# Optimization experiments

Measured on AMD Instinct MI355X. Metric: run time of the kernel, lower is better.

Reference implementation:

```python
import jax, jax.numpy as jnp
import numpy as np

EMBED_DIM = 1024
NUM_HEADS = 16
HEAD_DIM = EMBED_DIM // NUM_HEADS
BATCH = 2
SEQ = 2048


def setup_inputs() -> dict:
    key = jax.random.key(0)
    ks = jax.random.split(key, 9)
    s = EMBED_DIM ** -0.5
    inp = {"x": jax.random.normal(ks[0], (BATCH, SEQ, EMBED_DIM), dtype=jnp.float32)}
    names = ["Wq", "Wk", "Wv", "Wo"]
    for i, n in enumerate(names):
        inp[n] = jax.random.normal(ks[1 + i], (EMBED_DIM, EMBED_DIM), dtype=jnp.float32) * s
        inp["b" + n[1]] = jax.random.normal(ks[5 + i], (EMBED_DIM,), dtype=jnp.float32) * 0.02
    return inp


def reference(x, Wq, bq, Wk, bk, Wv, bv, Wo, bo):
    B, S, E = x.shape
    H, D = NUM_HEADS, HEAD_DIM
    scaling = D ** -0.5
    # projections (torch Linear: x @ W.T + b), reshape to (B, H, S, D)
    q = (x @ Wq.T + bq).reshape(B, S, H, D).transpose(0, 2, 1, 3)
    k = (x @ Wk.T + bk).reshape(B, S, H, D).transpose(0, 2, 1, 3)
    v = (x @ Wv.T + bv).reshape(B, S, H, D).transpose(0, 2, 1, 3)
    # full materialized score matrix, matching the original module
    scores = jnp.einsum("bhqd,bhkd->bhqk", q, k) * scaling
    causal = jnp.triu(jnp.ones((S, S), dtype=bool), k=1)  # True above diagonal
    scores = jnp.where(causal[None, None], -jnp.inf, scores)
    attn = jax.nn.softmax(scores, axis=-1)
    out = jnp.einsum("bhqk,bhkd->bhqd", attn, v)  # (B, H, S, D)
    out = out.transpose(0, 2, 1, 3).reshape(B, S, E)
    return out @ Wo.T + bo
```

## Files before the change

kernel.cpp:

```cpp
#include <hip/hip_runtime.h>
#include <stdint.h>

typedef __bf16 bf16;
typedef __bf16 bf16x8 __attribute__((ext_vector_type(8)));
typedef __bf16 bf16x4 __attribute__((ext_vector_type(4)));
typedef float  f32x4  __attribute__((ext_vector_type(4)));
typedef unsigned int u32;

#define E_DIM 1024
#define S_LEN 2048
#define BATCH 2
#define NH 16
#define DH 64

#define NEG_INF (-__builtin_inff())

union BU { u32 u[4]; bf16x8 h; };

__device__ __forceinline__ u32 cvtpk_bf16(float lo, float hi) {
    u32 r;
    asm("v_cvt_pk_bf16_f32 %0, %1, %2" : "=v"(r) : "v"(lo), "v"(hi));
    return r;
}
__device__ __forceinline__ void pswap32(u32 &a, u32 &b) {
    asm("v_permlane32_swap_b32 %0, %1" : "+v"(a), "+v"(b));
}
__device__ __forceinline__ void pswap16(u32 &a, u32 &b) {
    asm("v_permlane16_swap_b32 %0, %1" : "+v"(a), "+v"(b));
}
__device__ __forceinline__ float fast_exp2(float x) {
    float r;
    asm("v_exp_f32 %0, %1" : "=v"(r) : "v"(x));
    return r;
}

__device__ __forceinline__ void load_lds16(const bf16* g, bf16* l) {
    __builtin_amdgcn_global_load_lds(
        (const __attribute__((address_space(1))) void*)g,
        (__attribute__((address_space(3))) void*)l, 16, 0, 0);
}

__global__ __launch_bounds__(256) void convert_kernel(
    const float* __restrict__ s0, const float* __restrict__ s1,
    const float* __restrict__ s2, const float* __restrict__ s3,
    const float* __restrict__ s4,
    bf16* __restrict__ d0, bf16* __restrict__ d1, bf16* __restrict__ d2,
    bf16* __restrict__ d3, bf16* __restrict__ d4,
    int n0, int n1)
{
    const float* src; bf16* dst; int n;
    switch (blockIdx.y) {
        case 0:  src = s0; dst = d0; n = n0; break;
        case 1:  src = s1; dst = d1; n = n1; break;
        case 2:  src = s2; dst = d2; n = n1; break;
        case 3:  src = s3; dst = d3; n = n1; break;
        default: src = s4; dst = d4; n = n1; break;
    }
    int i = (blockIdx.x * 256 + threadIdx.x) * 4;
    if (i >= n) return;
    float4 v = *(const float4*)(src + i);
    bf16x4 o;
    o[0] = (bf16)v.x; o[1] = (bf16)v.y; o[2] = (bf16)v.z; o[3] = (bf16)v.w;
    *(bf16x4*)(dst + i) = o;
}

__global__ __launch_bounds__(256) void gemm_kernel(
    const bf16* __restrict__ A,
    const bf16* __restrict__ W,
    const float* __restrict__ bias0, const float* __restrict__ bias1,
    const float* __restrict__ bias2,
    bf16* __restrict__ outQ, bf16* __restrict__ outK, bf16* __restrict__ outVt,
    float* __restrict__ outF, int final_mode)
{
    __shared__ bf16 As[2][128 * 32];
    __shared__ bf16 Bs[2][128 * 32];

    const int bid = blockIdx.x;
    const int xcd = bid & 7, idx = bid >> 3;
    int mtile, ntile;
    if (final_mode) {
        mtile = (xcd >> 1) * 8 + (idx >> 2);
        ntile = (xcd & 1) * 4 + (idx & 3);
    } else {
        mtile = (xcd >> 1) * 8 + idx / 12;
        ntile = (xcd & 1) * 12 + idx % 12;
    }
    const int bm = mtile * 128, bn = ntile * 128;
    const int mode = final_mode ? 3 : (bn >> 10);
    const float* bias = (mode == 1) ? bias1 : (mode == 2 ? bias2 : bias0);

    const int t = threadIdx.x;
    const int lane = t & 63, w = t >> 6;
    const int quad = lane >> 4, l16 = lane & 15;
    const int wm = (w & 1) * 64, wn = (w >> 1) * 64;

    const int r0 = w * 16;
    const int srow = r0 + (lane >> 2);
    const int scol = ((lane & 3) ^ ((lane >> 3) & 3)) * 8;
    const bf16* Ag0 = A + (size_t)(bm + srow) * E_DIM + scol;
    const bf16* Ag1 = Ag0 + (size_t)64 * E_DIM;
    const bf16* Wg0 = W + (size_t)(bn + srow) * E_DIM + scol;
    const bf16* Wg1 = Wg0 + (size_t)64 * E_DIM;

    f32x4 acc[4][4];
#pragma unroll
    for (int i = 0; i < 4; i++)
#pragma unroll
        for (int j = 0; j < 4; j++) acc[i][j] = f32x4{0.f, 0.f, 0.f, 0.f};

    load_lds16(Ag0, As[0] + r0 * 32);
    load_lds16(Ag1, As[0] + (64 + r0) * 32);
    load_lds16(Wg0, Bs[0] + r0 * 32);
    load_lds16(Wg1, Bs[0] + (64 + r0) * 32);

    const int rchunk = (quad ^ ((l16 >> 1) & 3)) * 8;

    int cur = 0;
    for (int kt = 0; kt < E_DIM; kt += 32) {
        __syncthreads();

        if (kt + 32 < E_DIM) {
            const int nxt = cur ^ 1;
            load_lds16(Ag0 + kt + 32, As[nxt] + r0 * 32);
            load_lds16(Ag1 + kt + 32, As[nxt] + (64 + r0) * 32);
            load_lds16(Wg0 + kt + 32, Bs[nxt] + r0 * 32);
            load_lds16(Wg1 + kt + 32, Bs[nxt] + (64 + r0) * 32);
        }

        bf16x8 af[4], bfr[4];
#pragma unroll
        for (int i = 0; i < 4; i++)
            af[i] = *(const bf16x8*)(As[cur] + (wm + i * 16 + l16) * 32 + rchunk);
#pragma unroll
        for (int j = 0; j < 4; j++)
            bfr[j] = *(const bf16x8*)(Bs[cur] + (wn + j * 16 + l16) * 32 + rchunk);
#pragma unroll
        for (int i = 0; i < 4; i++)
#pragma unroll
            for (int j = 0; j < 4; j++)
                acc[i][j] = __builtin_amdgcn_mfma_f32_16x16x32_bf16(af[i], bfr[j], acc[i][j], 0, 0, 0);

        cur ^= 1;
    }

#pragma unroll
    for (int j = 0; j < 4; j++) {
        const int n = bn + wn + j * 16 + l16;
        const int nl = n & 1023;
        const float bv = bias[nl];
#pragma unroll
        for (int i = 0; i < 4; i++) {
            const int m0 = bm + wm + i * 16 + quad * 4;
            if (mode == 3) {
#pragma unroll
                for (int r = 0; r < 4; r++)
                    outF[(size_t)(m0 + r) * E_DIM + nl] = acc[i][j][r] + bv;
            } else if (mode == 2) {
                const int b_ = m0 >> 11, s0 = m0 & (S_LEN - 1);
                const int h = nl >> 6, d = nl & 63;
                bf16x4 pv;
#pragma unroll
                for (int r = 0; r < 4; r++) pv[r] = (bf16)(acc[i][j][r] + bv);
                *(bf16x4*)(outVt + ((size_t)((b_ * NH + h) * DH + d)) * S_LEN + s0) = pv;
            } else {
                bf16* o = (mode == 0) ? outQ : outK;
                const float sc = (mode == 0) ? 0.18033688f : 1.0f;
                const int h = nl >> 6, d = nl & 63;
#pragma unroll
                for (int r = 0; r < 4; r++) {
                    const int m = m0 + r;
                    const int b_ = m >> 11, s = m & (S_LEN - 1);
                    o[((size_t)(b_ * NH + h) * S_LEN + s) * DH + d] = (bf16)((acc[i][j][r] + bv) * sc);
                }
            }
        }
    }
}

__global__ __launch_bounds__(512, 4) void attn_kernel(
    const bf16* __restrict__ Qb, const bf16* __restrict__ Kb,
    const bf16* __restrict__ Vtb,
    float* __restrict__ Opart, float* __restrict__ Lpart)
{
    __shared__ __align__(16) char smem[35840];
    bf16* Ks = (bf16*)smem;
    bf16* Vs = (bf16*)(smem + 18432);

    const int t = threadIdx.x, lane = t & 63, w = t >> 6;
    const int quad = lane >> 4, l16 = lane & 15;
    const int qs = w & 3, kh = w >> 2;

    const int i = blockIdx.x;
    const int xcd = i & 7, idx = i >> 3;
    const int bh  = (xcd << 2) | (idx & 3);
    const int g   = idx >> 2;
    int qt, c0;
    if (g < 4)       { qt = g;                            c0 = 0; }
    else if (g < 12) { int u = g - 4;  qt = 4 + (u >> 1); c0 = u & 1; }
    else if (g < 24) { int u = g - 12; qt = 8 + u / 3;    c0 = u % 3; }
    else             { int u = g - 24; qt = 12 + (u >> 2); c0 = u & 3; }
    const int k0 = c0 * 4;
    const int k1 = (k0 + 3 < qt) ? k0 + 3 : qt;

    const bf16* Qg = Qb + (size_t)bh * S_LEN * DH;
    const bf16* Kg = Kb + (size_t)bh * S_LEN * DH;
    const bf16* Vg = Vtb + (size_t)bh * DH * S_LEN;
    float* Op = Opart + ((size_t)(bh * 16 + qt) * 4 + c0) * (128 * 64);
    float* Lp = Lpart + ((size_t)(bh * 16 + qt) * 4 + c0) * 128;

    const int qrow0 = qt * 128 + qs * 32;

    bf16x8 qf[2][2];
#pragma unroll
    for (int qh = 0; qh < 2; qh++) {
        const bf16* qp = Qg + (size_t)(qrow0 + qh * 16 + l16) * DH + quad * 8;
        qf[qh][0] = *(const bf16x8*)(qp);
        qf[qh][1] = *(const bf16x8*)(qp + 32);
    }

    f32x4 o[2][4];
    f32x4 lacc[2];
#pragma unroll
    for (int qh = 0; qh < 2; qh++) {
        lacc[qh] = f32x4{0.f, 0.f, 0.f, 0.f};
#pragma unroll
        for (int dt = 0; dt < 4; dt++) o[qh][dt] = f32x4{0.f, 0.f, 0.f, 0.f};
    }

    const int kr0 = t >> 3, kce = (t & 7) * 8;
    const int vr0 = t >> 4, vce = (t & 15) * 8;

    const int kb0 = k0 * 128;
    uint4 kA = *(const uint4*)(Kg + (size_t)(kb0 + kr0) * DH + kce);
    uint4 kB = *(const uint4*)(Kg + (size_t)(kb0 + kr0 + 64) * DH + kce);
    uint4 vA = *(const uint4*)(Vg + (size_t)vr0 * S_LEN + kb0 + vce);
    uint4 vB = *(const uint4*)(Vg + (size_t)(vr0 + 32) * S_LEN + kb0 + vce);

    for (int kt = k0; kt <= k1; kt++) {
        __syncthreads();
        *(uint4*)(Ks + kr0 * 72 + kce) = kA;
        *(uint4*)(Ks + (kr0 + 64) * 72 + kce) = kB;
        *(uint4*)(Vs + vr0 * 136 + vce) = vA;
        *(uint4*)(Vs + (vr0 + 32) * 136 + vce) = vB;
        __syncthreads();

        if (kt < k1) {
            const int kb = (kt + 1) * 128;
            kA = *(const uint4*)(Kg + (size_t)(kb + kr0) * DH + kce);
            kB = *(const uint4*)(Kg + (size_t)(kb + kr0 + 64) * DH + kce);
            vA = *(const uint4*)(Vg + (size_t)vr0 * S_LEN + kb + vce);
            vB = *(const uint4*)(Vg + (size_t)(vr0 + 32) * S_LEN + kb + vce);
        }

        const bool diag = (kt == qt);

#pragma unroll
        for (int itp = 0; itp < 2; itp++) {
            f32x4 p[2][2];
#pragma unroll
            for (int e = 0; e < 2; e++) {
                const int itg = kh * 4 + itp * 2 + e;
                const bf16* kp = Ks + (itg * 16 + l16) * 72 + quad * 8;
                bf16x8 kf0 = *(const bf16x8*)(kp);
                bf16x8 kf1 = *(const bf16x8*)(kp + 32);
#pragma unroll
                for (int qh = 0; qh < 2; qh++) {
                    f32x4 s = __builtin_amdgcn_mfma_f32_16x16x32_bf16(
                        kf0, qf[qh][0], f32x4{0.f, 0.f, 0.f, 0.f}, 0, 0, 0);
                    s = __builtin_amdgcn_mfma_f32_16x16x32_bf16(
                        kf1, qf[qh][1], s, 0, 0, 0);
                    if (diag) {
                        const int kloc = kh * 64 + (itp * 2 + e) * 16 + quad * 4;
                        const int qloc = qs * 32 + qh * 16 + l16;
#pragma unroll
                        for (int r = 0; r < 4; r++)
                            if (kloc + r > qloc) s[r] = NEG_INF;
                    }
                    f32x4 pe;
#pragma unroll
                    for (int r = 0; r < 4; r++) pe[r] = fast_exp2(s[r]);
                    lacc[qh] += pe;
                    p[qh][e] = pe;
                }
            }

            BU bu0, bu1;
            {
                u32 a0 = cvtpk_bf16(p[0][0][0], p[0][0][1]);
                u32 a1 = cvtpk_bf16(p[0][0][2], p[0][0][3]);
                u32 b0 = cvtpk_bf16(p[0][1][0], p[0][1][1]);
                u32 b1 = cvtpk_bf16(p[0][1][2], p[0][1][3]);
                pswap32(a0, b0); pswap16(a0, b0);
                pswap32(a1, b1); pswap16(a1, b1);
                bu0.u[0] = a0; bu0.u[1] = a1; bu0.u[2] = b0; bu0.u[3] = b1;
            }
            {
                u32 a0 = cvtpk_bf16(p[1][0][0], p[1][0][1]);
                u32 a1 = cvtpk_bf16(p[1][0][2], p[1][0][3]);
                u32 b0 = cvtpk_bf16(p[1][1][0], p[1][1][1]);
                u32 b1 = cvtpk_bf16(p[1][1][2], p[1][1][3]);
                pswap32(a0, b0); pswap16(a0, b0);
                pswap32(a1, b1); pswap16(a1, b1);
                bu1.u[0] = a0; bu1.u[1] = a1; bu1.u[2] = b0; bu1.u[3] = b1;
            }

            const int ksg = kh * 2 + itp;
#pragma unroll
            for (int dt = 0; dt < 4; dt++) {
                bf16x8 vf = *(const bf16x8*)(Vs + (dt * 16 + l16) * 136 + ksg * 32 + quad * 8);
                o[0][dt] = __builtin_amdgcn_mfma_f32_16x16x32_bf16(vf, bu0.h, o[0][dt], 0, 0, 0);
                o[1][dt] = __builtin_amdgcn_mfma_f32_16x16x32_bf16(vf, bu1.h, o[1][dt], 0, 0, 0);
            }
        }
    }

    float lsum[2];
#pragma unroll
    for (int qh = 0; qh < 2; qh++) {
        float l = lacc[qh][0] + lacc[qh][1] + lacc[qh][2] + lacc[qh][3];
        l += __shfl_xor(l, 16);
        l += __shfl_xor(l, 32);
        lsum[qh] = l;
    }

    __syncthreads();
    f32x4* Or = (f32x4*)smem;
    float*  Lr = (float*)(smem + 32768);

    if (kh == 1) {
#pragma unroll
        for (int qh = 0; qh < 2; qh++) {
#pragma unroll
            for (int dt = 0; dt < 4; dt++)
                Or[(((qs * 2 + qh) * 4 + dt) * 4 + quad) * 16 + l16] = o[qh][dt];
            if (quad == 0) Lr[(qs * 2 + qh) * 16 + l16] = lsum[qh];
        }
    }
    __syncthreads();
    if (kh == 0) {
#pragma unroll
        for (int qh = 0; qh < 2; qh++) {
            const float lc = lsum[qh] + Lr[(qs * 2 + qh) * 16 + l16];
            const int row = qs * 32 + qh * 16 + l16;
            if (quad == 0) Lp[row] = lc;
#pragma unroll
            for (int dt = 0; dt < 4; dt++) {
                f32x4 ov = o[qh][dt] + Or[(((qs * 2 + qh) * 4 + dt) * 4 + quad) * 16 + l16];
                *(f32x4*)(Op + (size_t)row * 64 + dt * 16 + quad * 4) = ov;
            }
        }
    }
}

__global__ __launch_bounds__(256) void norm_kernel(
    const float* __restrict__ Opart, const float* __restrict__ Lpart,
    bf16* __restrict__ Ab)
{
    const int j = (blockIdx.x * 256 + threadIdx.x) * 4;
    const int b = j >> 21, s = (j >> 10) & (S_LEN - 1), e = j & 1023;
    const int h = e >> 6, d = e & 63;
    const int bh = b * NH + h;
    const int qt = s >> 7, row = s & 127;
    const int nc = (qt >> 2) + 1;
    const float* Op = Opart + ((size_t)(bh * 16 + qt) * 4) * (128 * 64)
                    + (size_t)row * 64 + d;
    const float* Lp = Lpart + ((size_t)(bh * 16 + qt) * 4) * 128 + row;
    f32x4 ov = *(const f32x4*)Op;
    float l = Lp[0];
    for (int c = 1; c < nc; c++) {
        ov += *(const f32x4*)(Op + c * (128 * 64));
        l += Lp[c * 128];
    }
    const float inv = 1.0f / l;
    bf16x4 w4;
#pragma unroll
    for (int r = 0; r < 4; r++) w4[r] = (bf16)(ov[r] * inv);
    *(bf16x4*)(Ab + j) = w4;
}

extern "C" void kernel_launch(void* const* d_in, const int* in_sizes, int n_in,
                              void* d_out, int out_size, void* d_ws, size_t ws_size,
                              hipStream_t stream)
{
    const float* x  = (const float*)d_in[0];
    const float* Wq = (const float*)d_in[1];
    const float* bq = (const float*)d_in[2];
    const float* Wk = (const float*)d_in[3];
    const float* bk = (const float*)d_in[4];
    const float* Wv = (const float*)d_in[5];
    const float* bv = (const float*)d_in[6];
    const float* Wo = (const float*)d_in[7];
    const float* bo = (const float*)d_in[8];
    float* out = (float*)d_out;

    char* ws = (char*)d_ws;
    const size_t MB = 1ull << 20;
    bf16*  xb    = (bf16*)(ws + 0);
    bf16*  wqb   = (bf16*)(ws + 8 * MB);
    bf16*  wkb   = (bf16*)(ws + 10 * MB);
    bf16*  wvb   = (bf16*)(ws + 12 * MB);
    bf16*  wob   = (bf16*)(ws + 14 * MB);
    bf16*  Qb    = (bf16*)(ws + 16 * MB);
    bf16*  Kb    = (bf16*)(ws + 24 * MB);
    bf16*  Vtb   = (bf16*)(ws + 32 * MB);
    bf16*  Ab    = (bf16*)(ws + 40 * MB);
    float* Opart = (float*)(ws + 48 * MB);
    float* Lpart = (float*)(ws + 112 * MB);

    convert_kernel<<<dim3(4096, 5), 256, 0, stream>>>(
        x, Wq, Wk, Wv, Wo, xb, wqb, wkb, wvb, wob, 4194304, 1048576);

    gemm_kernel<<<dim3(768), 256, 0, stream>>>(
        xb, wqb, bq, bk, bv, Qb, Kb, Vtb, nullptr, 0);

    attn_kernel<<<dim3(1280), 512, 0, stream>>>(Qb, Kb, Vtb, Opart, Lpart);

    norm_kernel<<<dim3(4096), 256, 0, stream>>>(Opart, Lpart, Ab);

    gemm_kernel<<<dim3(256), 256, 0, stream>>>(
        Ab, wob, bo, bo, bo, nullptr, nullptr, nullptr, out, 1);
}
```

Baseline: 201.7 us.

## Use 256x256x64 tiled QKV projection GEMM with 512 threads and swizzled LDS

Adds a new QKV projection kernel that uses 256x256 output tiles with 64-wide K steps, 8 waves, XOR-swizzled LDS layout, direct global-to-LDS loads and s_setprio around the MFMA block. The aim is more data reuse per tile and fewer, larger K iterations for the 4096x3072x1024 GEMM. The original gemm kernel is reduced to the output projection only. Risks: 192 blocks on 256 CUs leaves some CUs idle, and 128KB of LDS plus a large accumulator may limit occupancy to one block per CU.

```diff
diff --git a/kernel.cpp b/kernel.cpp
--- a/kernel.cpp
+++ b/kernel.cpp
@@ -64,30 +64,137 @@
     *(bf16x4*)(dst + i) = o;
 }
 
-__global__ __launch_bounds__(256) void gemm_kernel(
+__global__ __launch_bounds__(512) void gemm256_kernel(
     const bf16* __restrict__ A,
     const bf16* __restrict__ W,
     const float* __restrict__ bias0, const float* __restrict__ bias1,
     const float* __restrict__ bias2,
-    bf16* __restrict__ outQ, bf16* __restrict__ outK, bf16* __restrict__ outVt,
-    float* __restrict__ outF, int final_mode)
+    bf16* __restrict__ outQ, bf16* __restrict__ outK, bf16* __restrict__ outVt)
+{
+    __shared__ bf16 As[2][256 * 64];
+    __shared__ bf16 Bs[2][256 * 64];
+
+    const int bid = blockIdx.x;
+    const int xcd = bid & 7, idx = bid >> 3;
+    const int mtile = (xcd >> 1) * 4 + idx / 6;
+    const int ntile = (xcd & 1) * 6 + idx % 6;
+    const int bm = mtile * 256, bn = ntile * 256;
+    const int mode = bn >> 10;
+    const float* bias = (mode == 1) ? bias1 : (mode == 2 ? bias2 : bias0);
+
+    const int t = threadIdx.x;
+    const int lane = t & 63, w = t >> 6;
+    const int quad = lane >> 4, l16 = lane & 15;
+    const int wrow = (w & 1) * 128, wcol = (w >> 1) * 64;
+
+    const int grow  = w * 8 + (lane >> 3);
+    const int gslot = (lane & 7) ^ ((lane >> 3) & 7);
+    const bf16* Ag = A + (size_t)(bm + grow) * E_DIM + gslot * 8;
+    const bf16* Wg = W + (size_t)(bn + grow) * E_DIM + gslot * 8;
+
+#define STAGE256(buf, kt) do {                                              \
+    const bf16* ag_ = Ag + (kt) * 64;                                       \
+    const bf16* wg_ = Wg + (kt) * 64;                                       \
+    bf16* la_ = As[buf] + w * 512;                                          \
+    bf16* lb_ = Bs[buf] + w * 512;                                          \
+    load_lds16(ag_,                 la_);                                   \
+    load_lds16(ag_ +  64 * E_DIM,   la_ + 4096);                            \
+    load_lds16(ag_ + 128 * E_DIM,   la_ + 8192);                            \
+    load_lds16(ag_ + 192 * E_DIM,   la_ + 12288);                           \
+    load_lds16(wg_,                 lb_);                                   \
+    load_lds16(wg_ +  64 * E_DIM,   lb_ + 4096);                            \
+    load_lds16(wg_ + 128 * E_DIM,   lb_ + 8192);                            \
+    load_lds16(wg_ + 192 * E_DIM,   lb_ + 12288);                           \
+} while (0)
+
+    f32x4 acc[8][4];
+#pragma unroll
+    for (int m = 0; m < 8; m++)
+#pragma unroll
+        for (int j = 0; j < 4; j++) acc[m][j] = f32x4{0.f, 0.f, 0.f, 0.f};
+
+    STAGE256(0, 0);
+
+    int cur = 0;
+    for (int i = 0; i < 16; i++) {
+        if (i < 15) {
+            STAGE256(cur ^ 1, i + 1);
+            asm volatile("s_waitcnt vmcnt(8)" ::: "memory");
+        } else {
+            asm volatile("s_waitcnt vmcnt(0)" ::: "memory");
+        }
+        __builtin_amdgcn_s_barrier();
+
+        __builtin_amdgcn_s_setprio(1);
+#pragma unroll
+        for (int ks = 0; ks < 2; ks++) {
+            bf16x8 bfr[4];
+#pragma unroll
+            for (int j = 0; j < 4; j++)
+                bfr[j] = *(const bf16x8*)(Bs[cur] + (wcol + j * 16 + l16) * 64
+                                          + (((ks * 4 + quad) ^ (l16 & 7)) * 8));
+#pragma unroll
+            for (int m = 0; m < 8; m++) {
+                bf16x8 af = *(const bf16x8*)(As[cur] + (wrow + m * 16 + l16) * 64
+                                             + (((ks * 4 + quad) ^ (l16 & 7)) * 8));
+#pragma unroll
+                for (int j = 0; j < 4; j++)
+                    acc[m][j] = __builtin_amdgcn_mfma_f32_16x16x32_bf16(af, bfr[j], acc[m][j], 0, 0, 0);
+            }
+        }
+        __builtin_amdgcn_s_setprio(0);
+
+        asm volatile("s_waitcnt lgkmcnt(0)" ::: "memory");
+        __builtin_amdgcn_s_barrier();
+        cur ^= 1;
+    }
+#undef STAGE256
+
+#pragma unroll
+    for (int j = 0; j < 4; j++) {
+        const int n = bn + wcol + j * 16 + l16;
+        const int nl = n & 1023;
+        const float bv = bias[nl];
+#pragma unroll
+        for (int m = 0; m < 8; m++) {
+            const int m0 = bm + wrow + m * 16 + quad * 4;
+            if (mode == 2) {
+                const int b_ = m0 >> 11, s0 = m0 & (S_LEN - 1);
+                const int h = nl >> 6, d = nl & 63;
+                bf16x4 pv;
+#pragma unroll
+                for (int r = 0; r < 4; r++) pv[r] = (bf16)(acc[m][j][r] + bv);
+                *(bf16x4*)(outVt + ((size_t)((b_ * NH + h) * DH + d)) * S_LEN + s0) = pv;
+            } else {
+                bf16* o = (mode == 0) ? outQ : outK;
+                const float sc = (mode == 0) ? 0.18033688f : 1.0f;
+                const int h = nl >> 6, d = nl & 63;
+#pragma unroll
+                for (int r = 0; r < 4; r++) {
+                    const int mm = m0 + r;
+                    const int b_ = mm >> 11, s = mm & (S_LEN - 1);
+                    o[((size_t)(b_ * NH + h) * S_LEN + s) * DH + d] = (bf16)((acc[m][j][r] + bv) * sc);
+                }
+            }
+        }
+    }
+}
+
+__global__ __launch_bounds__(256) void gemm_kernel(
+    const bf16* __restrict__ A,
+    const bf16* __restrict__ W,
+    const float* __restrict__ bias0,
+    float* __restrict__ outF)
 {
     __shared__ bf16 As[2][128 * 32];
     __shared__ bf16 Bs[2][128 * 32];
 
     const int bid = blockIdx.x;
     const int xcd = bid & 7, idx = bid >> 3;
-    int mtile, ntile;
-    if (final_mode) {
-        mtile = (xcd >> 1) * 8 + (idx >> 2);
-        ntile = (xcd & 1) * 4 + (idx & 3);
-    } else {
-        mtile = (xcd >> 1) * 8 + idx / 12;
-        ntile = (xcd & 1) * 12 + idx % 12;
-    }
+    const int mtile = (xcd >> 1) * 8 + (idx >> 2);
+    const int ntile = (xcd & 1) * 4 + (idx & 3);
     const int bm = mtile * 128, bn = ntile * 128;
-    const int mode = final_mode ? 3 : (bn >> 10);
-    const float* bias = (mode == 1) ? bias1 : (mode == 2 ? bias2 : bias0);
+    const float* bias = bias0;
 
     const int t = threadIdx.x;
     const int lane = t & 63, w = t >> 6;
@@ -146,33 +253,13 @@
 #pragma unroll
     for (int j = 0; j < 4; j++) {
         const int n = bn + wn + j * 16 + l16;
-        const int nl = n & 1023;
-        const float bv = bias[nl];
+        const float bv = bias[n];
 #pragma unroll
         for (int i = 0; i < 4; i++) {
             const int m0 = bm + wm + i * 16 + quad * 4;
-            if (mode == 3) {
-#pragma unroll
-                for (int r = 0; r < 4; r++)
-                    outF[(size_t)(m0 + r) * E_DIM + nl] = acc[i][j][r] + bv;
-            } else if (mode == 2) {
-                const int b_ = m0 >> 11, s0 = m0 & (S_LEN - 1);
-                const int h = nl >> 6, d = nl & 63;
-                bf16x4 pv;
-#pragma unroll
-                for (int r = 0; r < 4; r++) pv[r] = (bf16)(acc[i][j][r] + bv);
-                *(bf16x4*)(outVt + ((size_t)((b_ * NH + h) * DH + d)) * S_LEN + s0) = pv;
-            } else {
-                bf16* o = (mode == 0) ? outQ : outK;
-                const float sc = (mode == 0) ? 0.18033688f : 1.0f;
-                const int h = nl >> 6, d = nl & 63;
-#pragma unroll
-                for (int r = 0; r < 4; r++) {
-                    const int m = m0 + r;
-                    const int b_ = m >> 11, s = m & (S_LEN - 1);
-                    o[((size_t)(b_ * NH + h) * S_LEN + s) * DH + d] = (bf16)((acc[i][j][r] + bv) * sc);
-                }
-            }
+#pragma unroll
+            for (int r = 0; r < 4; r++)
+                outF[(size_t)(m0 + r) * E_DIM + n] = acc[i][j][r] + bv;
         }
     }
 }
@@ -410,13 +497,12 @@
     convert_kernel<<<dim3(4096, 5), 256, 0, stream>>>(
         x, Wq, Wk, Wv, Wo, xb, wqb, wkb, wvb, wob, 4194304, 1048576);
 
-    gemm_kernel<<<dim3(768), 256, 0, stream>>>(
-        xb, wqb, bq, bk, bv, Qb, Kb, Vtb, nullptr, 0);
+    gemm256_kernel<<<dim3(192), 512, 0, stream>>>(
+        xb, wqb, bq, bk, bv, Qb, Kb, Vtb);
 
     attn_kernel<<<dim3(1280), 512, 0, stream>>>(Qb, Kb, Vtb, Opart, Lpart);
 
     norm_kernel<<<dim3(4096), 256, 0, stream>>>(Opart, Lpart, Ab);
 
-    gemm_kernel<<<dim3(256), 256, 0, stream>>>(
-        Ab, wob, bo, bo, bo, nullptr, nullptr, nullptr, out, 1);
-}
+    gemm_kernel<<<dim3(256), 256, 0, stream>>>(Ab, wob, bo, out);
+}
```

Measured after the change: 196.0 us. -2.8%, faster.
